# Kernel tuning notes

Hardware: AMD Instinct MI355X
Metric: run time of the kernel (lower is better)

The kernel has to match this reference:

```python
import jax, jax.numpy as jnp
import numpy as np

N_NODES = 50000
N_EDGES = 800000
IN_CH = 512
HID = 256
HEADS = 8
OUT_CH = 64


def _glorot(key, shape):
    fan_in = shape[0] if len(shape) == 2 else shape[-1]
    return jax.random.normal(key, shape, jnp.float32) / jnp.sqrt(jnp.float32(fan_in))


def setup_inputs() -> dict:
    key = jax.random.key(0)
    ks = jax.random.split(key, 16)
    C = HID // HEADS  # 32, per-head dim
    return {
        "x": jax.random.normal(ks[0], (N_NODES, IN_CH), jnp.float32),
        "edge_index": jax.random.randint(ks[1], (2, N_EDGES), 0, N_NODES, jnp.int32),
        # layer 0: in -> heads*C, concat
        "W0": _glorot(ks[2], (IN_CH, HEADS * C)),
        "a_src0": _glorot(ks[3], (HEADS, C)),
        "a_dst0": _glorot(ks[4], (HEADS, C)),
        "b0": jnp.zeros((HEADS * C,), jnp.float32),
        # layer 1: hidden -> heads*C, concat
        "W1": _glorot(ks[5], (HID, HEADS * C)),
        "a_src1": _glorot(ks[6], (HEADS, C)),
        "a_dst1": _glorot(ks[7], (HEADS, C)),
        "b1": jnp.zeros((HEADS * C,), jnp.float32),
        # layer 2: hidden -> out_ch, 1 head, mean (concat=False)
        "W2": _glorot(ks[8], (HID, 1 * OUT_CH)),
        "a_src2": _glorot(ks[9], (1, OUT_CH)),
        "a_dst2": _glorot(ks[10], (1, OUT_CH)),
        "b2": jnp.zeros((OUT_CH,), jnp.float32),
    }


def gat_conv(x, W, a_src, a_dst, b, src, dst, concat):
    """PyG GATConv (self-loops already appended to src/dst), eval mode."""
    N = x.shape[0]
    H, C = a_src.shape
    h = (x @ W).reshape(N, H, C)                      # [N,H,C]
    alpha_src = jnp.sum(h * a_src, axis=-1)           # [N,H]
    alpha_dst = jnp.sum(h * a_dst, axis=-1)           # [N,H]
    e = jax.nn.leaky_relu(alpha_src[src] + alpha_dst[dst], 0.2)  # [E,H]
    # softmax over incoming edges per destination node
    m = jax.ops.segment_max(e, dst, num_segments=N)   # [N,H]
    m = jnp.where(jnp.isfinite(m), m, 0.0)
    w = jnp.exp(e - m[dst])
    s = jax.ops.segment_sum(w, dst, num_segments=N)
    alpha = w / (s[dst] + 1e-16)                      # [E,H]
    out = jax.ops.segment_sum(alpha[:, :, None] * h[src], dst, num_segments=N)
    out = out.reshape(N, H * C) if concat else out.mean(axis=1)
    return out + b


def reference(x, edge_index, W0, a_src0, a_dst0, b0, W1, a_src1, a_dst1, b1, W2, a_src2, a_dst2, b2):
    N = x.shape[0]
    loop = jnp.arange(N, dtype=edge_index.dtype)      # add_self_loops=True
    src = jnp.concatenate([edge_index[0], loop])
    dst = jnp.concatenate([edge_index[1], loop])
    # dropout is identity in eval mode
    h = jax.nn.elu(gat_conv(x, W0, a_src0, a_dst0, b0, src, dst, True))
    h = jax.nn.elu(gat_conv(h, W1, a_src1, a_dst1, b1, src, dst, True))
    h = gat_conv(h, W2, a_src2, a_dst2, b2, src, dst, False)
    return jax.nn.log_softmax(h, axis=1)
```

## Files before the change

### kernel.cpp

```cpp
#include <hip/hip_runtime.h>
#include <hip/hip_bf16.h>

typedef __attribute__((ext_vector_type(8))) short short8;
typedef __attribute__((ext_vector_type(4))) float f32x4;
typedef __attribute__((ext_vector_type(2))) float f32x2;
typedef __attribute__((ext_vector_type(4))) unsigned short us4;

__device__ __forceinline__ ushort f2bf(float f) {
    unsigned u = __float_as_uint(f);
    u += 0x7FFFu + ((u >> 16) & 1u);
    return (ushort)(u >> 16);
}
__device__ __forceinline__ float bf2f(ushort h) {
    return __uint_as_float(((unsigned)h) << 16);
}
__device__ __forceinline__ float lrelu(float e) { return (e >= 0.f) ? e : 0.2f * e; }
__device__ __forceinline__ unsigned char f2fp8(float v) {
    return (unsigned char)(__builtin_amdgcn_cvt_pk_fp8_f32(v, v, 0, false) & 0xFF);
}
__device__ __forceinline__ void gload16(const void* g, void* l) {
    __builtin_amdgcn_global_load_lds(
        (const __attribute__((address_space(1))) unsigned int*)g,
        (__attribute__((address_space(3))) unsigned int*)l, 16, 0, 0);
}

__global__ void k_scanA(const int* __restrict__ deg, int* __restrict__ bsum, int n) {
    __shared__ int sd[256];
    int t = blockIdx.x * 256 + threadIdx.x;
    sd[threadIdx.x] = (t < n) ? deg[t] + 1 : 0;
    __syncthreads();
    for (int off = 128; off > 0; off >>= 1) {
        if (threadIdx.x < off) sd[threadIdx.x] += sd[threadIdx.x + off];
        __syncthreads();
    }
    if (threadIdx.x == 0) bsum[blockIdx.x] = sd[0];
}
__global__ void k_scanC(const int* __restrict__ deg, const int* __restrict__ bsum,
                        int* __restrict__ rowptr, int* __restrict__ cursor,
                        int n, int etot, int nb) {
    __shared__ int sb[256];
    __shared__ int sd[256];
    __shared__ int sbx[256];
    int i = threadIdx.x;
    int bv = (i < nb) ? bsum[i] : 0;
    sb[i] = bv;
    __syncthreads();
    for (int off = 1; off < 256; off <<= 1) {
        int tv = (i >= off) ? sb[i - off] : 0;
        __syncthreads();
        sb[i] += tv;
        __syncthreads();
    }
    sbx[i] = sb[i] - bv;
    __syncthreads();
    int boff = sbx[blockIdx.x];

    int t = blockIdx.x * 256 + i;
    int v = (t < n) ? deg[t] + 1 : 0;
    sd[i] = v;
    __syncthreads();
    for (int off = 1; off < 256; off <<= 1) {
        int tv = (i >= off) ? sd[i - off] : 0;
        __syncthreads();
        sd[i] += tv;
        __syncthreads();
    }
    if (t < n) {
        int ex = boff + sd[i] - v;
        rowptr[t] = ex;
        cursor[t] = ex;
        if (t == n - 1) rowptr[n] = etot;
    }
}

__global__ void k_wh(const float* __restrict__ W0, ushort* __restrict__ T0,
                     const float* __restrict__ W1, ushort* __restrict__ T1,
                     const float* __restrict__ W2, ushort* __restrict__ T2,
                     const int* __restrict__ dst, int* __restrict__ deg, int e, int nhb) {
    if (blockIdx.x >= 832) {
        int hb = blockIdx.x - 832;
        int base = hb * 256 + threadIdx.x;
        int stride = nhb * 256;
#pragma unroll
        for (int k = 0; k < 4; ++k) {
            int i = base + k * stride;
            if (i < e) atomicAdd(&deg[dst[i]], 1);
        }
        return;
    }
    int i = blockIdx.x * blockDim.x + threadIdx.x;
    if (i < 131072) {
        int k = i >> 8, c = i & 255;
        T0[(size_t)c * 512 + k] = f2bf(W0[i]);
    } else if (i < 196608) {
        int j = i - 131072;
        int k = j >> 8, c = j & 255;
        T1[(size_t)c * 256 + k] = f2bf(W1[j]);
    } else if (i < 212992) {
        int j = i - 196608;
        int k = j >> 6, c = j & 63;
        T2[(size_t)c * 256 + k] = f2bf(W2[j]);
    }
}

__global__ __launch_bounds__(256) void k_g0s(const float* __restrict__ Ap,
                                             const ushort* __restrict__ BT,
                                             unsigned char* __restrict__ Cp,
                                             const float* __restrict__ asv,
                                             const float* __restrict__ adv,
                                             float* __restrict__ asrc,
                                             float* __restrict__ adst, int M,
                                             const int* __restrict__ ei,
                                             int* __restrict__ cursor,
                                             int* __restrict__ colb,
                                             int E, int nsb, int ngb) {
    constexpr int K = 512, BK = 32;
    constexpr int NK = K / BK;
    constexpr int AU = 256, BU = 512, TU = AU + BU;
    __shared__ __align__(16) ushort lds[2][TU * 8];

    const int bid = blockIdx.x;
    if ((bid & 3) == 3) {
        int sid = bid >> 2;
        if (sid < nsb) {
            int base = sid * 256 + threadIdx.x;
            int stride = nsb * 256;
            int etot = E + M;
#pragma unroll
            for (int k = 0; k < 4; ++k) {
                int i = base + k * stride;
                if (i < etot) {
                    int s, d;
                    if (i < E) { s = ei[i]; d = ei[E + i]; }
                    else       { s = i - E; d = s; }
                    int pos = atomicAdd(&cursor[d], 1);
                    colb[pos] = s;
                }
            }
        }
        return;
    }
    const int gb = bid - (bid >> 2);
    if (gb >= ngb) return;

    const int t = threadIdx.x;
    const int wid = t >> 6, lane = t & 63;
    const int lr = lane & 15, lg = lane >> 4;
    const int wm = wid >> 1, wn = wid & 1;
    const int bm0 = (gb >> 1) * 64;
    const int bn0 = (gb & 1) * 128;

    int a_off[2], b_off[4];
#pragma unroll
    for (int mf = 0; mf < 2; ++mf) {
        int row = wm * 32 + mf * 16 + lr;
        a_off[mf] = row * 64 + ((lg ^ ((row >> 1) & 3)) << 4);
    }
#pragma unroll
    for (int nf = 0; nf < 4; ++nf) {
        int col = wn * 64 + nf * 16 + lr;
        b_off[nf] = AU * 16 + col * 64 + ((lg ^ ((col >> 1) & 3)) << 4);
    }

    f32x4 acc[2][4];
#pragma unroll
    for (int mf = 0; mf < 2; ++mf)
#pragma unroll
        for (int nf = 0; nf < 4; ++nf) acc[mf][nf] = f32x4{0.f, 0.f, 0.f, 0.f};

    f32x4 ra[2];

    auto stage_B = [&](int buf, int kk) {
#pragma unroll
        for (int i = 0; i < 2; ++i) {
            int u = t + i * 256;
            int col = u >> 2;
            int g = (u & 3) ^ ((col >> 1) & 3);
            const ushort* src = BT + (size_t)(bn0 + col) * K + kk + g * 8;
            gload16(src, &lds[buf][(AU + u) * 8]);
        }
    };
    auto load_A32 = [&](int kk) {
        int u = t;
        int row = u >> 2;
        int g = (u & 3) ^ ((row >> 1) & 3);
        int grow = bm0 + row;
        if (grow >= M) grow = M - 1;
        const float* src = Ap + (size_t)grow * K + kk + g * 8;
        ra[0] = *(const f32x4*)src;
        ra[1] = *(const f32x4*)(src + 4);
    };
    auto write_A32 = [&](int buf) {
        short8 v;
#pragma unroll
        for (int j = 0; j < 4; ++j) {
            v[j] = (short)f2bf(ra[0][j]);
            v[4 + j] = (short)f2bf(ra[1][j]);
        }
        *(short8*)&lds[buf][t * 8] = v;
    };
    auto compute = [&](int buf) {
        const char* base = (const char*)lds[buf];
        short8 af[2], bf_[4];
#pragma unroll
        for (int mf = 0; mf < 2; ++mf) af[mf] = *(const short8*)(base + a_off[mf]);
#pragma unroll
        for (int nf = 0; nf < 4; ++nf) bf_[nf] = *(const short8*)(base + b_off[nf]);
#pragma unroll
        for (int mf = 0; mf < 2; ++mf)
#pragma unroll
            for (int nf = 0; nf < 4; ++nf)
                acc[mf][nf] = __builtin_amdgcn_mfma_f32_16x16x32_bf16(af[mf], bf_[nf], acc[mf][nf], 0, 0, 0);
    };

    load_A32(0);
    write_A32(0);
    stage_B(0, 0);
    __syncthreads();

    int buf = 0;
    for (int ks = 0; ks < NK; ++ks) {
        const int kk = (ks + 1) * BK;
        if (ks + 1 < NK) {
            load_A32(kk);
            stage_B(buf ^ 1, kk);
        }
        compute(buf);
        if (ks + 1 < NK) write_A32(buf ^ 1);
        __syncthreads();
        buf ^= 1;
    }

#pragma unroll
    for (int mf = 0; mf < 2; ++mf) {
#pragma unroll
        for (int nf = 0; nf < 4; ++nf) {
            int col = bn0 + wn * 64 + nf * 16 + lr;
#pragma unroll
            for (int p = 0; p < 4; ++p) {
                int row = bm0 + wm * 32 + mf * 16 + lg * 4 + p;
                if (row < M)
                    Cp[(size_t)row * 256 + col] = f2fp8(acc[mf][nf][p]);
            }
        }
    }

    {
        float cs[4], cd[4];
#pragma unroll
        for (int nf = 0; nf < 4; ++nf) {
            int col = bn0 + wn * 64 + nf * 16 + lr;
            cs[nf] = asv[col];
            cd[nf] = adv[col];
        }
        const int hb = (bn0 >> 5) + wn * 2;
#pragma unroll
        for (int mf = 0; mf < 2; ++mf) {
#pragma unroll
            for (int p = 0; p < 4; ++p) {
                float sA = acc[mf][0][p] * cs[0] + acc[mf][1][p] * cs[1];
                float sB = acc[mf][2][p] * cs[2] + acc[mf][3][p] * cs[3];
                float dA = acc[mf][0][p] * cd[0] + acc[mf][1][p] * cd[1];
                float dB = acc[mf][2][p] * cd[2] + acc[mf][3][p] * cd[3];
#pragma unroll
                for (int off = 1; off < 16; off <<= 1) {
                    sA += __shfl_xor(sA, off);
                    sB += __shfl_xor(sB, off);
                    dA += __shfl_xor(dA, off);
                    dB += __shfl_xor(dB, off);
                }
                int row = bm0 + wm * 32 + mf * 16 + lg * 4 + p;
                if (lr == 0 && row < M) {
                    asrc[row * 8 + hb] = sA;
                    asrc[row * 8 + hb + 1] = sB;
                    adst[row * 8 + hb] = dA;
                    adst[row * 8 + hb + 1] = dB;
                }
            }
        }
    }
}

template <int K, int BN>
__global__ __launch_bounds__(256) void k_gemm(const ushort* __restrict__ Ap,
                                              const ushort* __restrict__ BT,
                                              unsigned char* __restrict__ Cp,
                                              const float* __restrict__ asv,
                                              const float* __restrict__ adv,
                                              float* __restrict__ asrc,
                                              float* __restrict__ adst, int M) {
    constexpr int BM = 64, BK = 32;
    constexpr int NK = K / BK;
    constexpr int NF = BN / 32;
    constexpr int AU = BM * BK / 8;
    constexpr int BU = BN * BK / 8;
    constexpr int TU = AU + BU;
    __shared__ __align__(16) ushort lds[2][TU * 8];

    const int t = threadIdx.x;
    const int wid = t >> 6, lane = t & 63;
    const int lr = lane & 15, lg = lane >> 4;
    const int wm = wid >> 1, wn = wid & 1;
    const int bm0 = blockIdx.x * BM;
    const int bn0 = blockIdx.y * BN;
    const int Nc = BN * gridDim.y;

    int a_off[2], b_off[NF];
#pragma unroll
    for (int mf = 0; mf < 2; ++mf) {
        int row = wm * 32 + mf * 16 + lr;
        a_off[mf] = row * 64 + ((lg ^ ((row >> 1) & 3)) << 4);
    }
#pragma unroll
    for (int nf = 0; nf < NF; ++nf) {
        int col = wn * (BN / 2) + nf * 16 + lr;
        b_off[nf] = AU * 16 + col * 64 + ((lg ^ ((col >> 1) & 3)) << 4);
    }

    f32x4 acc[2][NF];
#pragma unroll
    for (int mf = 0; mf < 2; ++mf)
#pragma unroll
        for (int nf = 0; nf < NF; ++nf) acc[mf][nf] = f32x4{0.f, 0.f, 0.f, 0.f};

    auto stage_B = [&](int buf, int kk) {
#pragma unroll
        for (int i = 0; i < 2; ++i) {
            int u = t + i * 256;
            int col = u >> 2;
            int g = (u & 3) ^ ((col >> 1) & 3);
            const ushort* src = BT + (size_t)(bn0 + col) * K + kk + g * 8;
            gload16(src, &lds[buf][(AU + u) * 8]);
        }
    };
    auto stage_A16 = [&](int buf, int kk) {
        int u = t;
        int row = u >> 2;
        int g = (u & 3) ^ ((row >> 1) & 3);
        int grow = bm0 + row;
        if (grow >= M) grow = M - 1;
        const ushort* src = Ap + (size_t)grow * K + kk + g * 8;
        gload16(src, &lds[buf][u * 8]);
    };
    auto compute = [&](int buf) {
        const char* base = (const char*)lds[buf];
        short8 af[2], bf_[NF];
#pragma unroll
        for (int mf = 0; mf < 2; ++mf) af[mf] = *(const short8*)(base + a_off[mf]);
#pragma unroll
        for (int nf = 0; nf < NF; ++nf) bf_[nf] = *(const short8*)(base + b_off[nf]);
#pragma unroll
        for (int mf = 0; mf < 2; ++mf)
#pragma unroll
            for (int nf = 0; nf < NF; ++nf)
                acc[mf][nf] = __builtin_amdgcn_mfma_f32_16x16x32_bf16(af[mf], bf_[nf], acc[mf][nf], 0, 0, 0);
    };

    stage_A16(0, 0);
    stage_B(0, 0);
    __syncthreads();

    int buf = 0;
    for (int ks = 0; ks < NK; ++ks) {
        const int kk = (ks + 1) * BK;
        if (ks + 1 < NK) {
            stage_A16(buf ^ 1, kk);
            stage_B(buf ^ 1, kk);
        }
        compute(buf);
        __syncthreads();
        buf ^= 1;
    }

#pragma unroll
    for (int mf = 0; mf < 2; ++mf) {
#pragma unroll
        for (int nf = 0; nf < NF; ++nf) {
            int col = bn0 + wn * (BN / 2) + nf * 16 + lr;
#pragma unroll
            for (int p = 0; p < 4; ++p) {
                int row = bm0 + wm * 32 + mf * 16 + lg * 4 + p;
                if (row < M)
                    Cp[(size_t)row * Nc + col] = f2fp8(acc[mf][nf][p]);
            }
        }
    }

    if constexpr (NF == 4) {
        float cs[4], cd[4];
#pragma unroll
        for (int nf = 0; nf < 4; ++nf) {
            int col = bn0 + wn * 64 + nf * 16 + lr;
            cs[nf] = asv[col];
            cd[nf] = adv[col];
        }
        const int hb = (bn0 >> 5) + wn * 2;
#pragma unroll
        for (int mf = 0; mf < 2; ++mf) {
#pragma unroll
            for (int p = 0; p < 4; ++p) {
                float sA = acc[mf][0][p] * cs[0] + acc[mf][1][p] * cs[1];
                float sB = acc[mf][2][p] * cs[2] + acc[mf][3][p] * cs[3];
                float dA = acc[mf][0][p] * cd[0] + acc[mf][1][p] * cd[1];
                float dB = acc[mf][2][p] * cd[2] + acc[mf][3][p] * cd[3];
#pragma unroll
                for (int off = 1; off < 16; off <<= 1) {
                    sA += __shfl_xor(sA, off);
                    sB += __shfl_xor(sB, off);
                    dA += __shfl_xor(dA, off);
                    dB += __shfl_xor(dB, off);
                }
                int row = bm0 + wm * 32 + mf * 16 + lg * 4 + p;
                if (lr == 0 && row < M) {
                    asrc[row * 8 + hb] = sA;
                    asrc[row * 8 + hb + 1] = sB;
                    adst[row * 8 + hb] = dA;
                    adst[row * 8 + hb + 1] = dB;
                }
            }
        }
    }
}

__global__ __launch_bounds__(256) void k_gemm2(const ushort* __restrict__ Ap,
                                               const ushort* __restrict__ BT,
                                               ushort* __restrict__ Cp,
                                               const float* __restrict__ asv,
                                               const float* __restrict__ adv,
                                               float* __restrict__ asrc,
                                               float* __restrict__ adst, int M) {
    constexpr int K = 256, BM = 64, BK = 32;
    constexpr int NK = K / BK;
    constexpr int BU = 64 * BK / 8;
    constexpr int AU = BM * BK / 8;
    constexpr int TU = AU + BU;
    __shared__ __align__(16) ushort lds[2][TU * 8];

    const int t = threadIdx.x;
    const int wid = t >> 6, lane = t & 63;
    const int lr = lane & 15, lg = lane >> 4;
    const int bm0 = blockIdx.x * BM;

    int a_off0, b_off[4];
    {
        int row = wid * 16 + lr;
        a_off0 = row * 64 + ((lg ^ ((row >> 1) & 3)) << 4);
    }
#pragma unroll
    for (int nf = 0; nf < 4; ++nf) {
        int col = nf * 16 + lr;
        b_off[nf] = AU * 16 + col * 64 + ((lg ^ ((col >> 1) & 3)) << 4);
    }

    f32x4 acc[4];
#pragma unroll
    for (int nf = 0; nf < 4; ++nf) acc[nf] = f32x4{0.f, 0.f, 0.f, 0.f};

    auto stage_B = [&](int buf, int kk) {
        int u = t;
        int col = u >> 2;
        int g = (u & 3) ^ ((col >> 1) & 3);
        const ushort* src = BT + (size_t)col * K + kk + g * 8;
        gload16(src, &lds[buf][(AU + u) * 8]);
    };
    auto stage_A = [&](int buf, int kk) {
        int u = t;
        int row = u >> 2;
        int g = (u & 3) ^ ((row >> 1) & 3);
        int grow = bm0 + row;
        if (grow >= M) grow = M - 1;
        const ushort* src = Ap + (size_t)grow * K + kk + g * 8;
        gload16(src, &lds[buf][u * 8]);
    };
    auto compute = [&](int buf) {
        const char* base = (const char*)lds[buf];
        short8 af = *(const short8*)(base + a_off0);
        short8 bf_[4];
#pragma unroll
        for (int nf = 0; nf < 4; ++nf) bf_[nf] = *(const short8*)(base + b_off[nf]);
#pragma unroll
        for (int nf = 0; nf < 4; ++nf)
            acc[nf] = __builtin_amdgcn_mfma_f32_16x16x32_bf16(af, bf_[nf], acc[nf], 0, 0, 0);
    };

    stage_A(0, 0);
    stage_B(0, 0);
    __syncthreads();
    int buf = 0;
    for (int ks = 0; ks < NK; ++ks) {
        if (ks + 1 < NK) {
            stage_A(buf ^ 1, (ks + 1) * BK);
            stage_B(buf ^ 1, (ks + 1) * BK);
        }
        compute(buf);
        __syncthreads();
        buf ^= 1;
    }

    float cs[4], cd[4];
#pragma unroll
    for (int nf = 0; nf < 4; ++nf) {
        cs[nf] = asv[nf * 16 + lr];
        cd[nf] = adv[nf * 16 + lr];
    }
#pragma unroll
    for (int p = 0; p < 4; ++p) {
        int row = bm0 + wid * 16 + lg * 4 + p;
#pragma unroll
        for (int nf = 0; nf < 4; ++nf) {
            if (row < M)
                Cp[(size_t)row * 64 + nf * 16 + lr] = f2bf(acc[nf][p]);
        }
        float sA = acc[0][p] * cs[0] + acc[1][p] * cs[1] +
                   acc[2][p] * cs[2] + acc[3][p] * cs[3];
        float dA = acc[0][p] * cd[0] + acc[1][p] * cd[1] +
                   acc[2][p] * cd[2] + acc[3][p] * cd[3];
#pragma unroll
        for (int off = 1; off < 16; off <<= 1) {
            sA += __shfl_xor(sA, off);
            dA += __shfl_xor(dA, off);
        }
        if (lr == 0 && row < M) {
            asrc[row] = sA;
            adst[row] = dA;
        }
    }
}

#define MAXW 96
__global__ __launch_bounds__(128) void k_agg(const unsigned char* __restrict__ h8,
                                             const float* __restrict__ asrc,
                                             const float* __restrict__ adst,
                                             const int* __restrict__ rowptr,
                                             const int* __restrict__ col,
                                             const float* __restrict__ bias,
                                             ushort* __restrict__ anext, int n) {
    __shared__ float wl[2][MAXW * 8];
    int wid = threadIdx.x >> 6;
    int lane = threadIdx.x & 63;
    int node = blockIdx.x * 2 + wid;
    if (node >= n) return;
    int beg = rowptr[node], end = rowptr[node + 1];
    int deg = end - beg;
    int hd = lane >> 3;
    int eo = lane & 7;
    float ad = adst[node * 8 + hd];
    float* wp = wl[wid];

    float sacc = 0.f;
    for (int jb = eo; jb < deg; jb += 8) {
        int s = col[beg + jb];
        float w = __expf(lrelu(asrc[s * 8 + hd] + ad));
        if (jb < MAXW) wp[jb * 8 + hd] = w;
        sacc += w;
    }
    sacc += __shfl_xor(sacc, 1);
    sacc += __shfl_xor(sacc, 2);
    sacc += __shfl_xor(sacc, 4);
    float inv = 1.f / (sacc + 1e-16f);

    int nl = (deg < MAXW) ? deg : MAXW;
    float a0 = 0.f, a1 = 0.f, a2 = 0.f, a3 = 0.f;
    int jb = 0;
    for (; jb + 8 <= nl; jb += 8) {
        int sv[8];
#pragma unroll
        for (int i = 0; i < 8; ++i) sv[i] = col[beg + jb + i];
        unsigned gv[8];
#pragma unroll
        for (int i = 0; i < 8; ++i) gv[i] = *(const unsigned*)(h8 + (size_t)sv[i] * 256 + lane * 4);
        float wv[8];
#pragma unroll
        for (int i = 0; i < 8; ++i) wv[i] = wp[(jb + i) * 8 + hd];
#pragma unroll
        for (int i = 0; i < 8; ++i) {
            a0 += wv[i] * __builtin_amdgcn_cvt_f32_fp8(gv[i], 0);
            a1 += wv[i] * __builtin_amdgcn_cvt_f32_fp8(gv[i], 1);
            a2 += wv[i] * __builtin_amdgcn_cvt_f32_fp8(gv[i], 2);
            a3 += wv[i] * __builtin_amdgcn_cvt_f32_fp8(gv[i], 3);
        }
    }
    for (; jb < nl; ++jb) {
        int s = col[beg + jb];
        unsigned g = *(const unsigned*)(h8 + (size_t)s * 256 + lane * 4);
        float w = wp[jb * 8 + hd];
        a0 += w * __builtin_amdgcn_cvt_f32_fp8(g, 0);
        a1 += w * __builtin_amdgcn_cvt_f32_fp8(g, 1);
        a2 += w * __builtin_amdgcn_cvt_f32_fp8(g, 2);
        a3 += w * __builtin_amdgcn_cvt_f32_fp8(g, 3);
    }
    for (; jb < deg; ++jb) {
        int s = col[beg + jb];
        unsigned g = *(const unsigned*)(h8 + (size_t)s * 256 + lane * 4);
        float w = __expf(lrelu(asrc[s * 8 + hd] + ad));
        a0 += w * __builtin_amdgcn_cvt_f32_fp8(g, 0);
        a1 += w * __builtin_amdgcn_cvt_f32_fp8(g, 1);
        a2 += w * __builtin_amdgcn_cvt_f32_fp8(g, 2);
        a3 += w * __builtin_amdgcn_cvt_f32_fp8(g, 3);
    }
    f32x4 bv = *(const f32x4*)(bias + lane * 4);
    float v0 = a0 * inv + bv[0];
    float v1 = a1 * inv + bv[1];
    float v2 = a2 * inv + bv[2];
    float v3 = a3 * inv + bv[3];
    v0 = (v0 > 0.f) ? v0 : expm1f(v0);
    v1 = (v1 > 0.f) ? v1 : expm1f(v1);
    v2 = (v2 > 0.f) ? v2 : expm1f(v2);
    v3 = (v3 > 0.f) ? v3 : expm1f(v3);
    us4 o;
    o[0] = f2bf(v0); o[1] = f2bf(v1); o[2] = f2bf(v2); o[3] = f2bf(v3);
    *(us4*)(anext + (size_t)node * 256 + lane * 4) = o;
}

__global__ __launch_bounds__(128) void k_agg2(const ushort* __restrict__ h2,
                                              const float* __restrict__ asrc,
                                              const float* __restrict__ adst,
                                              const int* __restrict__ rowptr,
                                              const int* __restrict__ col,
                                              const float* __restrict__ bias,
                                              float* __restrict__ out, int n) {
    int wid = threadIdx.x >> 6;
    int lane = threadIdx.x & 63;
    int node = blockIdx.x * 2 + wid;
    if (node >= n) return;
    int beg = rowptr[node], end = rowptr[node + 1];
    int deg = end - beg;
    float ad = adst[node];
    int g = lane >> 3;
    int ch = (lane & 7) * 8;

    f32x2 acc2[4];
#pragma unroll
    for (int i = 0; i < 4; ++i) acc2[i] = f32x2{0.f, 0.f};
    float ssum = 0.f;
    for (int p = 0; p < deg; p += 8) {
        int jb = p + g;
        float w = 0.f;
        uint4 gv = {0u, 0u, 0u, 0u};
        if (jb < deg) {
            int s = col[beg + jb];
            gv = *(const uint4*)(h2 + (size_t)s * 64 + ch);
            w = __expf(lrelu(asrc[s] + ad));
        }
        ssum += w;
        f32x2 w2 = {w, w};
        f32x2 p0 = {__uint_as_float(gv.x << 16), __uint_as_float(gv.x & 0xFFFF0000u)};
        f32x2 p1 = {__uint_as_float(gv.y << 16), __uint_as_float(gv.y & 0xFFFF0000u)};
        f32x2 p2 = {__uint_as_float(gv.z << 16), __uint_as_float(gv.z & 0xFFFF0000u)};
        f32x2 p3 = {__uint_as_float(gv.w << 16), __uint_as_float(gv.w & 0xFFFF0000u)};
        acc2[0] += w2 * p0;
        acc2[1] += w2 * p1;
        acc2[2] += w2 * p2;
        acc2[3] += w2 * p3;
    }
    float v[8];
#pragma unroll
    for (int i = 0; i < 4; ++i) { v[2 * i] = acc2[i].x; v[2 * i + 1] = acc2[i].y; }
#pragma unroll
    for (int off = 8; off < 64; off <<= 1) {
        ssum += __shfl_xor(ssum, off);
#pragma unroll
        for (int i = 0; i < 8; ++i) v[i] += __shfl_xor(v[i], off);
    }
    float inv = 1.f / (ssum + 1e-16f);
#pragma unroll
    for (int i = 0; i < 8; ++i) v[i] = v[i] * inv + bias[ch + i];
    float mx = v[0];
#pragma unroll
    for (int i = 1; i < 8; ++i) mx = fmaxf(mx, v[i]);
    mx = fmaxf(mx, __shfl_xor(mx, 1));
    mx = fmaxf(mx, __shfl_xor(mx, 2));
    mx = fmaxf(mx, __shfl_xor(mx, 4));
    float se = 0.f;
#pragma unroll
    for (int i = 0; i < 8; ++i) se += __expf(v[i] - mx);
    se += __shfl_xor(se, 1);
    se += __shfl_xor(se, 2);
    se += __shfl_xor(se, 4);
    float ls = mx + logf(se);
    if (g == 0) {
        f32x4 o0, o1;
#pragma unroll
        for (int i = 0; i < 4; ++i) { o0[i] = v[i] - ls; o1[i] = v[4 + i] - ls; }
        *(f32x4*)(out + (size_t)node * 64 + ch) = o0;
        *(f32x4*)(out + (size_t)node * 64 + ch + 4) = o1;
    }
}

extern "C" void kernel_launch(void* const* d_in, const int* in_sizes, int n_in,
                              void* d_out, int out_size, void* d_ws, size_t ws_size,
                              hipStream_t stream) {
    const float* x   = (const float*)d_in[0];
    const int*   ei  = (const int*)d_in[1];
    const float* W0  = (const float*)d_in[2];
    const float* as0 = (const float*)d_in[3];
    const float* ad0 = (const float*)d_in[4];
    const float* b0  = (const float*)d_in[5];
    const float* W1  = (const float*)d_in[6];
    const float* as1 = (const float*)d_in[7];
    const float* ad1 = (const float*)d_in[8];
    const float* b1  = (const float*)d_in[9];
    const float* W2  = (const float*)d_in[10];
    const float* as2 = (const float*)d_in[11];
    const float* ad2 = (const float*)d_in[12];
    const float* b2  = (const float*)d_in[13];
    float* out = (float*)d_out;

    const int N = in_sizes[0] / 512;
    const int E = in_sizes[1] / 2;
    const int ETOT = E + N;

    char* ws = (char*)d_ws;
    size_t off = 0;
    auto alloc = [&](size_t bytes) -> void* {
        off = (off + 255) & ~(size_t)255;
        void* p = ws + off;
        off += bytes;
        return p;
    };
    int* rowptr = (int*)alloc((size_t)(N + 1) * 4);
    int* cursor = (int*)alloc((size_t)N * 4);
    int* deg    = (int*)alloc((size_t)N * 4);
    int* bsum   = (int*)alloc(1024);
    int* colb   = (int*)alloc((size_t)ETOT * 4);
    ushort* WT0 = (ushort*)alloc((size_t)256 * 512 * 2);
    ushort* WT1 = (ushort*)alloc((size_t)256 * 256 * 2);
    ushort* WT2 = (ushort*)alloc((size_t)64 * 256 * 2);
    unsigned char* h8 = (unsigned char*)alloc((size_t)N * 256);
    ushort* abf = (ushort*)alloc((size_t)N * 256 * 2);
    float* asrc = (float*)alloc((size_t)N * 8 * 4);
    float* adst = (float*)alloc((size_t)N * 8 * 4);
    ushort* h2   = (ushort*)h8;
    float* asrc2 = asrc;
    float* adst2 = adst;

    const int nblk = (N + 255) / 256;
    const int nhb  = (E + 1023) / 1024;
    const int nsb  = (ETOT + 1023) / 1024;

    hipMemsetAsync(deg, 0, (size_t)N * 4, stream);
    k_wh<<<832 + nhb, 256, 0, stream>>>(W0, WT0, W1, WT1, W2, WT2, ei + E, deg, E, nhb);

    k_scanA<<<nblk, 256, 0, stream>>>(deg, bsum, N);
    k_scanC<<<nblk, 256, 0, stream>>>(deg, bsum, rowptr, cursor, N, ETOT, nblk);

    const int gblk = (N + 63) / 64;
    const int ngb  = 2 * gblk;
    const int ablk = (N + 1) / 2;

    const int fatT = 4 * nsb;
    k_g0s<<<fatT, 256, 0, stream>>>(x, WT0, h8, as0, ad0, asrc, adst, N,
                                    ei, cursor, colb, E, nsb, ngb);
    k_agg<<<ablk, 128, 0, stream>>>(h8, asrc, adst, rowptr, colb, b0, abf, N);

    k_gemm<256, 128><<<dim3(gblk, 2), 256, 0, stream>>>(abf, WT1, h8, as1, ad1, asrc, adst, N);
    k_agg<<<ablk, 128, 0, stream>>>(h8, asrc, adst, rowptr, colb, b1, abf, N);

    k_gemm2<<<gblk, 256, 0, stream>>>(abf, WT2, h2, as2, ad2, asrc2, adst2, N);
    k_agg2<<<ablk, 128, 0, stream>>>(h2, asrc2, adst2, rowptr, colb, b2, out, N);
}
```

Before: 297.2 us.

## Overlap second-half layer-0 aggregation with first-half layer-1 GEMM in fused kernel

Layer-0 aggregation is split at a row boundary. The first half runs alone. The second half then runs in a combined kernel where every eighth block does a layer-1 GEMM tile on the already-finished first-half rows, and a separate GEMM launch finishes the rest. This meant to fill idle compute during the memory-bound gather with MFMA work and to cut the serial gap between stages. Separate h8 and attention-score buffers are added so that the concurrent reads and writes do not conflict, at the cost of an extra launch and more workspace.

```diff
diff --git a/kernel.cpp b/kernel.cpp
--- a/kernel.cpp
+++ b/kernel.cpp
@@ -23,6 +23,8 @@
         (const __attribute__((address_space(1))) unsigned int*)g,
         (__attribute__((address_space(3))) unsigned int*)l, 16, 0, 0);
 }
+
+#define MAXW 96
 
 __global__ void k_scanA(const int* __restrict__ deg, int* __restrict__ bsum, int n) {
     __shared__ int sd[256];
@@ -103,6 +105,85 @@
     }
 }
 
+__device__ __forceinline__ void agg_node(const unsigned char* __restrict__ h8,
+                                         const float* __restrict__ asrc,
+                                         const float* __restrict__ adst,
+                                         const int* __restrict__ rowptr,
+                                         const int* __restrict__ col,
+                                         const float* __restrict__ bias,
+                                         ushort* __restrict__ anext,
+                                         int node, int lane, float* wp) {
+    int beg = rowptr[node], end = rowptr[node + 1];
+    int deg = end - beg;
+    int hd = lane >> 3;
+    int eo = lane & 7;
+    float ad = adst[node * 8 + hd];
+
+    float sacc = 0.f;
+    for (int jb = eo; jb < deg; jb += 8) {
+        int s = col[beg + jb];
+        float w = __expf(lrelu(asrc[s * 8 + hd] + ad));
+        if (jb < MAXW) wp[jb * 8 + hd] = w;
+        sacc += w;
+    }
+    sacc += __shfl_xor(sacc, 1);
+    sacc += __shfl_xor(sacc, 2);
+    sacc += __shfl_xor(sacc, 4);
+    float inv = 1.f / (sacc + 1e-16f);
+
+    int nl = (deg < MAXW) ? deg : MAXW;
+    float a0 = 0.f, a1 = 0.f, a2 = 0.f, a3 = 0.f;
+    int jb = 0;
+    for (; jb + 8 <= nl; jb += 8) {
+        int sv[8];
+#pragma unroll
+        for (int i = 0; i < 8; ++i) sv[i] = col[beg + jb + i];
+        unsigned gv[8];
+#pragma unroll
+        for (int i = 0; i < 8; ++i) gv[i] = *(const unsigned*)(h8 + (size_t)sv[i] * 256 + lane * 4);
+        float wv[8];
+#pragma unroll
+        for (int i = 0; i < 8; ++i) wv[i] = wp[(jb + i) * 8 + hd];
+#pragma unroll
+        for (int i = 0; i < 8; ++i) {
+            a0 += wv[i] * __builtin_amdgcn_cvt_f32_fp8(gv[i], 0);
+            a1 += wv[i] * __builtin_amdgcn_cvt_f32_fp8(gv[i], 1);
+            a2 += wv[i] * __builtin_amdgcn_cvt_f32_fp8(gv[i], 2);
+            a3 += wv[i] * __builtin_amdgcn_cvt_f32_fp8(gv[i], 3);
+        }
+    }
+    for (; jb < nl; ++jb) {
+        int s = col[beg + jb];
+        unsigned g = *(const unsigned*)(h8 + (size_t)s * 256 + lane * 4);
+        float w = wp[jb * 8 + hd];
+        a0 += w * __builtin_amdgcn_cvt_f32_fp8(g, 0);
+        a1 += w * __builtin_amdgcn_cvt_f32_fp8(g, 1);
+        a2 += w * __builtin_amdgcn_cvt_f32_fp8(g, 2);
+        a3 += w * __builtin_amdgcn_cvt_f32_fp8(g, 3);
+    }
+    for (; jb < deg; ++jb) {
+        int s = col[beg + jb];
+        unsigned g = *(const unsigned*)(h8 + (size_t)s * 256 + lane * 4);
+        float w = __expf(lrelu(asrc[s * 8 + hd] + ad));
+        a0 += w * __builtin_amdgcn_cvt_f32_fp8(g, 0);
+        a1 += w * __builtin_amdgcn_cvt_f32_fp8(g, 1);
+        a2 += w * __builtin_amdgcn_cvt_f32_fp8(g, 2);
+        a3 += w * __builtin_amdgcn_cvt_f32_fp8(g, 3);
+    }
+    f32x4 bv = *(const f32x4*)(bias + lane * 4);
+    float v0 = a0 * inv + bv[0];
+    float v1 = a1 * inv + bv[1];
+    float v2 = a2 * inv + bv[2];
+    float v3 = a3 * inv + bv[3];
+    v0 = (v0 > 0.f) ? v0 : expm1f(v0);
+    v1 = (v1 > 0.f) ? v1 : expm1f(v1);
+    v2 = (v2 > 0.f) ? v2 : expm1f(v2);
+    v3 = (v3 > 0.f) ? v3 : expm1f(v3);
+    us4 o;
+    o[0] = f2bf(v0); o[1] = f2bf(v1); o[2] = f2bf(v2); o[3] = f2bf(v3);
+    *(us4*)(anext + (size_t)node * 256 + lane * 4) = o;
+}
+
 __global__ __launch_bounds__(256) void k_g0s(const float* __restrict__ Ap,
                                              const ushort* __restrict__ BT,
                                              unsigned char* __restrict__ Cp,
@@ -281,47 +362,41 @@
     }
 }
 
-template <int K, int BN>
-__global__ __launch_bounds__(256) void k_gemm(const ushort* __restrict__ Ap,
-                                              const ushort* __restrict__ BT,
-                                              unsigned char* __restrict__ Cp,
-                                              const float* __restrict__ asv,
-                                              const float* __restrict__ adv,
-                                              float* __restrict__ asrc,
-                                              float* __restrict__ adst, int M) {
-    constexpr int BM = 64, BK = 32;
+__device__ __forceinline__ void gemm1_block(const ushort* __restrict__ Ap,
+                                            const ushort* __restrict__ BT,
+                                            unsigned char* __restrict__ Cp,
+                                            const float* __restrict__ asv,
+                                            const float* __restrict__ adv,
+                                            float* __restrict__ asrc,
+                                            float* __restrict__ adst, int M,
+                                            int bm0, int bn0, ushort* lds_raw) {
+    constexpr int K = 256, BK = 32;
     constexpr int NK = K / BK;
-    constexpr int NF = BN / 32;
-    constexpr int AU = BM * BK / 8;
-    constexpr int BU = BN * BK / 8;
-    constexpr int TU = AU + BU;
-    __shared__ __align__(16) ushort lds[2][TU * 8];
+    constexpr int AU = 256, BU = 512, TU = AU + BU;
+    ushort (*lds)[TU * 8] = (ushort (*)[TU * 8])lds_raw;
 
     const int t = threadIdx.x;
     const int wid = t >> 6, lane = t & 63;
     const int lr = lane & 15, lg = lane >> 4;
     const int wm = wid >> 1, wn = wid & 1;
-    const int bm0 = blockIdx.x * BM;
-    const int bn0 = blockIdx.y * BN;
-    const int Nc = BN * gridDim.y;
-
-    int a_off[2], b_off[NF];
+
+    int a_off[2], b_off[4];
 #pragma unroll
     for (int mf = 0; mf < 2; ++mf) {
         int row = wm * 32 + mf * 16 + lr;
         a_off[mf] = row * 64 + ((lg ^ ((row >> 1) & 3)) << 4);
     }
 #pragma unroll
-    for (int nf = 0; nf < NF; ++nf) {
-        int col = wn * (BN / 2) + nf * 16 + lr;
+    for (int nf = 0; nf < 4; ++nf) {
+        int col = wn * 64 + nf * 16 + lr;
         b_off[nf] = AU * 16 + col * 64 + ((lg ^ ((col >> 1) & 3)) << 4);
     }
 
-    f32x4 acc[2][NF];
+    f32x4 acc[2][4];
 #pragma unroll
     for (int mf = 0; mf < 2; ++mf)
 #pragma unroll
-        for (int nf = 0; nf < NF; ++nf) acc[mf][nf] = f32x4{0.f, 0.f, 0.f, 0.f};
+        for (int nf = 0; nf < 4; ++nf) acc[mf][nf] = f32x4{0.f, 0.f, 0.f, 0.f};
 
     auto stage_B = [&](int buf, int kk) {
 #pragma unroll
@@ -344,22 +419,21 @@
     };
     auto compute = [&](int buf) {
         const char* base = (const char*)lds[buf];
-        short8 af[2], bf_[NF];
+        short8 af[2], bf_[4];
 #pragma unroll
         for (int mf = 0; mf < 2; ++mf) af[mf] = *(const short8*)(base + a_off[mf]);
 #pragma unroll
-        for (int nf = 0; nf < NF; ++nf) bf_[nf] = *(const short8*)(base + b_off[nf]);
+        for (int nf = 0; nf < 4; ++nf) bf_[nf] = *(const short8*)(base + b_off[nf]);
 #pragma unroll
         for (int mf = 0; mf < 2; ++mf)
 #pragma unroll
-            for (int nf = 0; nf < NF; ++nf)
+            for (int nf = 0; nf < 4; ++nf)
                 acc[mf][nf] = __builtin_amdgcn_mfma_f32_16x16x32_bf16(af[mf], bf_[nf], acc[mf][nf], 0, 0, 0);
     };
 
     stage_A16(0, 0);
     stage_B(0, 0);
     __syncthreads();
-
     int buf = 0;
     for (int ks = 0; ks < NK; ++ks) {
         const int kk = (ks + 1) * BK;
@@ -375,18 +449,18 @@
 #pragma unroll
     for (int mf = 0; mf < 2; ++mf) {
 #pragma unroll
-        for (int nf = 0; nf < NF; ++nf) {
-            int col = bn0 + wn * (BN / 2) + nf * 16 + lr;
+        for (int nf = 0; nf < 4; ++nf) {
+            int col = bn0 + wn * 64 + nf * 16 + lr;
 #pragma unroll
             for (int p = 0; p < 4; ++p) {
                 int row = bm0 + wm * 32 + mf * 16 + lg * 4 + p;
                 if (row < M)
-                    Cp[(size_t)row * Nc + col] = f2fp8(acc[mf][nf][p]);
+                    Cp[(size_t)row * 256 + col] = f2fp8(acc[mf][nf][p]);
             }
         }
     }
 
-    if constexpr (NF == 4) {
+    {
         float cs[4], cd[4];
 #pragma unroll
         for (int nf = 0; nf < 4; ++nf) {
@@ -422,6 +496,65 @@
     }
 }
 
+__global__ __launch_bounds__(128) void k_agg(const unsigned char* __restrict__ h8,
+                                             const float* __restrict__ asrc,
+                                             const float* __restrict__ adst,
+                                             const int* __restrict__ rowptr,
+                                             const int* __restrict__ col,
+                                             const float* __restrict__ bias,
+                                             ushort* __restrict__ anext, int n0, int n1) {
+    __shared__ float wl[2][MAXW * 8];
+    int wid = threadIdx.x >> 6;
+    int lane = threadIdx.x & 63;
+    int node = n0 + blockIdx.x * 2 + wid;
+    if (node >= n1) return;
+    agg_node(h8, asrc, adst, rowptr, col, bias, anext, node, lane, wl[wid]);
+}
+
+__global__ __launch_bounds__(256) void k_a1g1(const unsigned char* __restrict__ h8a,
+                                              const float* __restrict__ asrc0,
+                                              const float* __restrict__ adst0,
+                                              const int* __restrict__ rowptr,
+                                              const int* __restrict__ col,
+                                              const float* __restrict__ bias0,
+                                              ushort* __restrict__ abf,
+                                              const ushort* __restrict__ BT1,
+                                              unsigned char* __restrict__ h8b,
+                                              const float* __restrict__ asv1,
+                                              const float* __restrict__ adv1,
+                                              float* __restrict__ asrc1,
+                                              float* __restrict__ adst1,
+                                              int M, int n0, int ngb) {
+    __shared__ __align__(16) ushort lds[2][768 * 8];
+    const int bid = blockIdx.x;
+    if ((bid & 7) == 7) {
+        int gid = bid >> 3;
+        if (gid < ngb)
+            gemm1_block(abf, BT1, h8b, asv1, adv1, asrc1, adst1, M,
+                        (gid >> 1) * 64, (gid & 1) * 128, &lds[0][0]);
+        return;
+    }
+    int aid = bid - (bid >> 3);
+    int wid = threadIdx.x >> 6;
+    int lane = threadIdx.x & 63;
+    int node = n0 + aid * 4 + wid;
+    if (node >= M) return;
+    float* wp = (float*)&lds[0][0] + wid * (MAXW * 8);
+    agg_node(h8a, asrc0, adst0, rowptr, col, bias0, abf, node, lane, wp);
+}
+
+__global__ __launch_bounds__(256) void k_gemm1(const ushort* __restrict__ Ap,
+                                               const ushort* __restrict__ BT,
+                                               unsigned char* __restrict__ Cp,
+                                               const float* __restrict__ asv,
+                                               const float* __restrict__ adv,
+                                               float* __restrict__ asrc,
+                                               float* __restrict__ adst, int M, int R0) {
+    __shared__ __align__(16) ushort lds[2][768 * 8];
+    gemm1_block(Ap, BT, Cp, asv, adv, asrc, adst, M,
+                R0 + blockIdx.x * 64, blockIdx.y * 128, &lds[0][0]);
+}
+
 __global__ __launch_bounds__(256) void k_gemm2(const ushort* __restrict__ Ap,
                                                const ushort* __restrict__ BT,
                                                ushort* __restrict__ Cp,
@@ -525,91 +658,6 @@
             adst[row] = dA;
         }
     }
-}
-
-#define MAXW 96
-__global__ __launch_bounds__(128) void k_agg(const unsigned char* __restrict__ h8,
-                                             const float* __restrict__ asrc,
-                                             const float* __restrict__ adst,
-                                             const int* __restrict__ rowptr,
-                                             const int* __restrict__ col,
-                                             const float* __restrict__ bias,
-                                             ushort* __restrict__ anext, int n) {
-    __shared__ float wl[2][MAXW * 8];
-    int wid = threadIdx.x >> 6;
-    int lane = threadIdx.x & 63;
-    int node = blockIdx.x * 2 + wid;
-    if (node >= n) return;
-    int beg = rowptr[node], end = rowptr[node + 1];
-    int deg = end - beg;
-    int hd = lane >> 3;
-    int eo = lane & 7;
-    float ad = adst[node * 8 + hd];
-    float* wp = wl[wid];
-
-    float sacc = 0.f;
-    for (int jb = eo; jb < deg; jb += 8) {
-        int s = col[beg + jb];
-        float w = __expf(lrelu(asrc[s * 8 + hd] + ad));
-        if (jb < MAXW) wp[jb * 8 + hd] = w;
-        sacc += w;
-    }
-    sacc += __shfl_xor(sacc, 1);
-    sacc += __shfl_xor(sacc, 2);
-    sacc += __shfl_xor(sacc, 4);
-    float inv = 1.f / (sacc + 1e-16f);
-
-    int nl = (deg < MAXW) ? deg : MAXW;
-    float a0 = 0.f, a1 = 0.f, a2 = 0.f, a3 = 0.f;
-    int jb = 0;
-    for (; jb + 8 <= nl; jb += 8) {
-        int sv[8];
-#pragma unroll
-        for (int i = 0; i < 8; ++i) sv[i] = col[beg + jb + i];
-        unsigned gv[8];
-#pragma unroll
-        for (int i = 0; i < 8; ++i) gv[i] = *(const unsigned*)(h8 + (size_t)sv[i] * 256 + lane * 4);
-        float wv[8];
-#pragma unroll
-        for (int i = 0; i < 8; ++i) wv[i] = wp[(jb + i) * 8 + hd];
-#pragma unroll
-        for (int i = 0; i < 8; ++i) {
-            a0 += wv[i] * __builtin_amdgcn_cvt_f32_fp8(gv[i], 0);
-            a1 += wv[i] * __builtin_amdgcn_cvt_f32_fp8(gv[i], 1);
-            a2 += wv[i] * __builtin_amdgcn_cvt_f32_fp8(gv[i], 2);
-            a3 += wv[i] * __builtin_amdgcn_cvt_f32_fp8(gv[i], 3);
-        }
-    }
-    for (; jb < nl; ++jb) {
-        int s = col[beg + jb];
-        unsigned g = *(const unsigned*)(h8 + (size_t)s * 256 + lane * 4);
-        float w = wp[jb * 8 + hd];
-        a0 += w * __builtin_amdgcn_cvt_f32_fp8(g, 0);
-        a1 += w * __builtin_amdgcn_cvt_f32_fp8(g, 1);
-        a2 += w * __builtin_amdgcn_cvt_f32_fp8(g, 2);
-        a3 += w * __builtin_amdgcn_cvt_f32_fp8(g, 3);
-    }
-    for (; jb < deg; ++jb) {
-        int s = col[beg + jb];
-        unsigned g = *(const unsigned*)(h8 + (size_t)s * 256 + lane * 4);
-        float w = __expf(lrelu(asrc[s * 8 + hd] + ad));
-        a0 += w * __builtin_amdgcn_cvt_f32_fp8(g, 0);
-        a1 += w * __builtin_amdgcn_cvt_f32_fp8(g, 1);
-        a2 += w * __builtin_amdgcn_cvt_f32_fp8(g, 2);
-        a3 += w * __builtin_amdgcn_cvt_f32_fp8(g, 3);
-    }
-    f32x4 bv = *(const f32x4*)(bias + lane * 4);
-    float v0 = a0 * inv + bv[0];
-    float v1 = a1 * inv + bv[1];
-    float v2 = a2 * inv + bv[2];
-    float v3 = a3 * inv + bv[3];
-    v0 = (v0 > 0.f) ? v0 : expm1f(v0);
-    v1 = (v1 > 0.f) ? v1 : expm1f(v1);
-    v2 = (v2 > 0.f) ? v2 : expm1f(v2);
-    v3 = (v3 > 0.f) ? v3 : expm1f(v3);
-    us4 o;
-    o[0] = f2bf(v0); o[1] = f2bf(v1); o[2] = f2bf(v2); o[3] = f2bf(v3);
-    *(us4*)(anext + (size_t)node * 256 + lane * 4) = o;
 }
 
 __global__ __launch_bounds__(128) void k_agg2(const ushort* __restrict__ h2,
@@ -709,6 +757,7 @@
     const int N = in_sizes[0] / 512;
     const int E = in_sizes[1] / 2;
     const int ETOT = E + N;
+    const int HALF = 25024;
 
     char* ws = (char*)d_ws;
     size_t off = 0;
@@ -726,13 +775,16 @@
     ushort* WT0 = (ushort*)alloc((size_t)256 * 512 * 2);
     ushort* WT1 = (ushort*)alloc((size_t)256 * 256 * 2);
     ushort* WT2 = (ushort*)alloc((size_t)64 * 256 * 2);
-    unsigned char* h8 = (unsigned char*)alloc((size_t)N * 256);
+    unsigned char* h8a = (unsigned char*)alloc((size_t)N * 256);
+    unsigned char* h8b = (unsigned char*)alloc((size_t)N * 256);
     ushort* abf = (ushort*)alloc((size_t)N * 256 * 2);
-    float* asrc = (float*)alloc((size_t)N * 8 * 4);
-    float* adst = (float*)alloc((size_t)N * 8 * 4);
-    ushort* h2   = (ushort*)h8;
-    float* asrc2 = asrc;
-    float* adst2 = adst;
+    float* asrc0 = (float*)alloc((size_t)N * 8 * 4);
+    float* adst0 = (float*)alloc((size_t)N * 8 * 4);
+    float* asrc1 = (float*)alloc((size_t)N * 8 * 4);
+    float* adst1 = (float*)alloc((size_t)N * 8 * 4);
+    ushort* h2   = (ushort*)h8a;
+    float* asrc2 = asrc0;
+    float* adst2 = adst0;
 
     const int nblk = (N + 255) / 256;
     const int nhb  = (E + 1023) / 1024;
@@ -746,16 +798,29 @@
 
     const int gblk = (N + 63) / 64;
     const int ngb  = 2 * gblk;
-    const int ablk = (N + 1) / 2;
-
-    const int fatT = 4 * nsb;
-    k_g0s<<<fatT, 256, 0, stream>>>(x, WT0, h8, as0, ad0, asrc, adst, N,
-                                    ei, cursor, colb, E, nsb, ngb);
-    k_agg<<<ablk, 128, 0, stream>>>(h8, asrc, adst, rowptr, colb, b0, abf, N);
-
-    k_gemm<256, 128><<<dim3(gblk, 2), 256, 0, stream>>>(abf, WT1, h8, as1, ad1, asrc, adst, N);
-    k_agg<<<ablk, 128, 0, stream>>>(h8, asrc, adst, rowptr, colb, b1, abf, N);
+    const int hblk = HALF / 64;
+
+    k_g0s<<<4 * nsb, 256, 0, stream>>>(x, WT0, h8a, as0, ad0, asrc0, adst0, N,
+                                       ei, cursor, colb, E, nsb, ngb);
+
+    k_agg<<<HALF / 2, 128, 0, stream>>>(h8a, asrc0, adst0, rowptr, colb, b0, abf, 0, HALF);
+
+    {
+        const int aggBlocks = (N - HALF + 3) / 4;
+        const int gHalf = 2 * hblk;
+        int T = aggBlocks + gHalf;
+        while ((T >> 3) < gHalf || T - ((T + 0) / 8) < aggBlocks + ((T % 8) == 0 ? 0 : 0)) T++;
+        T = (aggBlocks * 8 + 6) / 7;
+        if ((T >> 3) < gHalf) T = gHalf * 8;
+        k_a1g1<<<T + 8, 256, 0, stream>>>(h8a, asrc0, adst0, rowptr, colb, b0, abf,
+                                          WT1, h8b, as1, ad1, asrc1, adst1, N, HALF, gHalf);
+    }
+
+    k_gemm1<<<dim3(gblk - hblk, 2), 256, 0, stream>>>(abf, WT1, h8b, as1, ad1,
+                                                      asrc1, adst1, N, HALF);
+
+    k_agg<<<(N + 1) / 2, 128, 0, stream>>>(h8b, asrc1, adst1, rowptr, colb, b1, abf, 0, N);
 
     k_gemm2<<<gblk, 256, 0, stream>>>(abf, WT2, h2, as2, ad2, asrc2, adst2, N);
-    k_agg2<<<ablk, 128, 0, stream>>>(h2, asrc2, adst2, rowptr, colb, b2, out, N);
-}
+    k_agg2<<<(N + 1) / 2, 128, 0, stream>>>(h2, asrc2, adst2, rowptr, colb, b2, out, N);
+}
```

Result: slower. 330.1 us (+11.1%).
